# Optimization experiments

Measured on AMD Instinct MI355X. Metric: run time of the kernel, lower is better.

Reference implementation:

```python
import jax, jax.numpy as jnp
import numpy as np

B, L, CH = 8, 32768, 128   # segments, points per segment, channels
H, D = 4, 32               # num_head, ch_head (CH == H*D)
EPS = 1e-5                 # torch GroupNorm default eps


def group_norm1(x, w, b):
    # GroupNorm(num_groups=1, num_channels=CH) applied on [1, CH, L] per segment:
    # normalize over all channels AND points of each segment, then per-channel affine.
    mu = jnp.mean(x, axis=(1, 2), keepdims=True)            # [B,1,1]
    var = jnp.var(x, axis=(1, 2), keepdims=True)            # [B,1,1]
    return (x - mu) * jax.lax.rsqrt(var + EPS) * w + b      # [B,L,CH]


def setup_inputs() -> dict:
    key = jax.random.key(0)
    k0, k1, k2 = jax.random.split(key, 3)
    x = jax.random.normal(k0, (B, L, CH), dtype=jnp.float32)
    W_qkv = jax.random.normal(k1, (CH, 3 * H * D), dtype=jnp.float32) * 0.02
    W_out = jax.random.normal(k2, (H * D, CH), dtype=jnp.float32) * 0.02
    gn1_w = jnp.ones((CH,), jnp.float32)
    gn1_b = jnp.zeros((CH,), jnp.float32)
    gn2_w = jnp.ones((CH,), jnp.float32)
    gn2_b = jnp.zeros((CH,), jnp.float32)
    return {"x": x, "gn1_w": gn1_w, "gn1_b": gn1_b, "W_qkv": W_qkv,
            "W_out": W_out, "gn2_w": gn2_w, "gn2_b": gn2_b}


def reference(x, gn1_w, gn1_b, W_qkv, W_out, gn2_w, gn2_b):
    norm_x = group_norm1(x, gn1_w, gn1_b)                     # [B,L,CH]
    qkv = norm_x @ W_qkv                                      # [B,L,3*H*D]
    q, k, v = jnp.split(qkv, 3, axis=-1)
    q = q.reshape(B, L, H, D)
    k = k.reshape(B, L, H, D)
    v = v.reshape(B, L, H, D)
    # softmax over points within each segment (k / sqrt(segment_len))
    k_soft = jax.nn.softmax(k * (1.0 / np.float32(np.sqrt(L))), axis=1)
    # per-segment, per-head KV context: [B,H,D,D]
    context = jnp.einsum('blhk,blhv->bhkv', k_soft, v)
    # q scaled by ch_head**-0.5, softmax over feature dim
    q_soft = jax.nn.softmax(q * np.float32(D ** -0.5), axis=-1)
    out = jnp.einsum('blhk,bhkv->blhv', q_soft, context).reshape(B, L, H * D)
    out = out @ W_out                                          # [B,L,CH]
    out = group_norm1(out, gn2_w, gn2_b)
    return out + x  # residual
```

## Files before the change

kernel.cpp:

```cpp
#include <hip/hip_runtime.h>

#define NSEG 8
#define LSEG 32768
#define EPS_GN 1e-5f
#define KSCALE 0.005524271728019903f
#define QSCALE 0.17677669529663687f
#define INVN 2.384185791015625e-07f

typedef __attribute__((ext_vector_type(4))) float f32x4;
typedef __attribute__((ext_vector_type(8))) __bf16 bf16x8;
typedef __attribute__((ext_vector_type(4))) short s16x4;

#define MFMA32(A, B, C) __builtin_amdgcn_mfma_f32_16x16x32_bf16(A, B, C, 0, 0, 0)
#define MFMA16(A, B, C) __builtin_amdgcn_mfma_f32_16x16x16bf16_1k(A, B, C, 0, 0, 0)

static __device__ __forceinline__ unsigned short f2bf(float f) {
  unsigned int u = __float_as_uint(f);
  u += 0x7fffu + ((u >> 16) & 1u);
  return (unsigned short)(u >> 16);
}
static __device__ __forceinline__ float bf2f(unsigned short s) {
  return __uint_as_float(((unsigned int)s) << 16);
}
static __device__ __forceinline__ s16x4 pack4(float a, float b, float c, float d) {
  union { __bf16 h[4]; s16x4 s; } u;
  u.h[0] = (__bf16)a; u.h[1] = (__bf16)b; u.h[2] = (__bf16)c; u.h[3] = (__bf16)d;
  return u.s;
}

__global__ __launch_bounds__(256) void k_pre(
    const float* __restrict__ x, float* __restrict__ part, unsigned short* __restrict__ xb,
    const float* __restrict__ W, const float* __restrict__ gn1w, unsigned short* __restrict__ WT)
{
  const int t = threadIdx.x;
  if (blockIdx.x >= 512) {
    int idx = (blockIdx.x - 512) * 256 + t;
    int n = idx >> 7, ch = idx & 127;
    WT[idx] = f2bf(gn1w[ch] * W[ch * 384 + n]);
    return;
  }
  const int c = blockIdx.x;
  const float4* xp = (const float4*)x + (size_t)c * 16384;
  ushort4* xo = (ushort4*)xb + (size_t)c * 16384;
  float s = 0.f, q = 0.f;
  for (int i = 0; i < 64; ++i) {
    float4 v = xp[t + i * 256];
    s += v.x + v.y + v.z + v.w;
    q += v.x*v.x + v.y*v.y + v.z*v.z + v.w*v.w;
    xo[t + i * 256] = make_ushort4(f2bf(v.x), f2bf(v.y), f2bf(v.z), f2bf(v.w));
  }
  #pragma unroll
  for (int o = 1; o < 64; o <<= 1) { s += __shfl_xor(s, o); q += __shfl_xor(q, o); }
  __shared__ float red[8];
  int wave = t >> 6, lane = t & 63;
  if (lane == 0) { red[wave*2] = s; red[wave*2+1] = q; }
  __syncthreads();
  if (t == 0) {
    part[c*2]   = red[0] + red[2] + red[4] + red[6];
    part[c*2+1] = red[1] + red[3] + red[5] + red[7];
  }
}

__global__ __launch_bounds__(256, 2) void k_kv(
    const unsigned short* __restrict__ xb, const unsigned short* __restrict__ WT,
    const float* __restrict__ Wqkv, const float* __restrict__ gn1w, const float* __restrict__ gn1b,
    const float* __restrict__ part, float* __restrict__ sume_p, float* __restrict__ ctx_p)
{
  __shared__ float sm[2];
  __shared__ float sb01[512];
  __shared__ float sbias[256];

  const int t = threadIdx.x;
  const int h = t >> 6, lane = t & 63;
  const int lm = lane & 15, lg = lane >> 4;
  const int bid = blockIdx.x;
  const int seg = bid >> 6, sub = bid & 63;

  if (t < 64) {
    float s = part[(seg*64 + t)*2], q = part[(seg*64 + t)*2 + 1];
    #pragma unroll
    for (int o = 1; o < 64; o <<= 1) { s += __shfl_xor(s, o); q += __shfl_xor(q, o); }
    if (t == 0) {
      float mu = s * INVN;
      float var = q * INVN - mu * mu;
      float rs = rsqrtf(var + EPS_GN);
      sm[0] = mu * rs; sm[1] = rs;
    }
  }
  for (int p = t; p < 512; p += 256) {
    int which = p >> 8, n = 128 + (p & 255);
    const float* gv = which ? gn1w : gn1b;
    float s = 0.f;
    for (int ch = 0; ch < 128; ++ch) s += gv[ch] * Wqkv[ch*384 + n];
    sb01[p] = s;
  }
  __syncthreads();
  {
    float mu_rs = sm[0];
    int p = t;
    float v = sb01[p] - mu_rs * sb01[256 + p];
    sbias[p] = v * ((p < 128) ? KSCALE : 1.f);
  }
  __syncthreads();

  const float rs = sm[1];
  const float alk = rs * KSCALE, alv = rs;
  const float ck0 = sbias[h*32 + lm],       ck1 = sbias[h*32 + 16 + lm];
  const float cv0 = sbias[128 + h*32 + lm], cv1 = sbias[128 + h*32 + 16 + lm];

  bf16x8 wk[2][4], wv[2][4];
  #pragma unroll
  for (int nt = 0; nt < 2; ++nt)
    #pragma unroll
    for (int kk = 0; kk < 4; ++kk) {
      int row = h*32 + nt*16 + lm;
      wk[nt][kk] = *(const bf16x8*)&WT[(row + 128) * 128 + kk*32 + lg*8];
      wv[nt][kk] = *(const bf16x8*)&WT[(row + 256) * 128 + kk*32 + lg*8];
    }

  f32x4 ctx00 = {0,0,0,0}, ctx01 = {0,0,0,0}, ctx10 = {0,0,0,0}, ctx11 = {0,0,0,0};
  float se0 = 0.f, se1 = 0.f;

  const unsigned short* xw = xb + (size_t)(seg * LSEG + sub*512 + lm) * 128 + lg*8;

#define ISSUE(S, IT) { \
    const unsigned short* p_ = xw + (size_t)((IT) * 16) * 128; \
    S[0] = *(const bf16x8*)(p_);      \
    S[1] = *(const bf16x8*)(p_ + 32); \
    S[2] = *(const bf16x8*)(p_ + 64); \
    S[3] = *(const bf16x8*)(p_ + 96); }

#define COMPUTE(S) { \
    f32x4 ka0 = {0,0,0,0}, ka1 = {0,0,0,0}, va0 = {0,0,0,0}, va1 = {0,0,0,0}; \
    _Pragma("unroll") for (int kk = 0; kk < 4; ++kk) { \
      ka0 = MFMA32(S[kk], wk[0][kk], ka0); \
      ka1 = MFMA32(S[kk], wk[1][kk], ka1); \
    } \
    _Pragma("unroll") for (int kk = 0; kk < 4; ++kk) { \
      va0 = MFMA32(S[kk], wv[0][kk], va0); \
      va1 = MFMA32(S[kk], wv[1][kk], va1); \
    } \
    float e_[8]; \
    _Pragma("unroll") for (int r = 0; r < 4; ++r) { \
      e_[r]     = __expf(fmaf(ka0[r], alk, ck0)); \
      e_[4 + r] = __expf(fmaf(ka1[r], alk, ck1)); \
    } \
    se0 += (e_[0] + e_[1]) + (e_[2] + e_[3]); \
    se1 += (e_[4] + e_[5]) + (e_[6] + e_[7]); \
    s16x4 E0 = pack4(e_[0], e_[1], e_[2], e_[3]); \
    s16x4 E1 = pack4(e_[4], e_[5], e_[6], e_[7]); \
    s16x4 V0 = pack4(fmaf(va0[0], alv, cv0), fmaf(va0[1], alv, cv0), \
                     fmaf(va0[2], alv, cv0), fmaf(va0[3], alv, cv0)); \
    s16x4 V1 = pack4(fmaf(va1[0], alv, cv1), fmaf(va1[1], alv, cv1), \
                     fmaf(va1[2], alv, cv1), fmaf(va1[3], alv, cv1)); \
    ctx00 = MFMA16(E0, V0, ctx00); \
    ctx01 = MFMA16(E0, V1, ctx01); \
    ctx10 = MFMA16(E1, V0, ctx10); \
    ctx11 = MFMA16(E1, V1, ctx11); }

  bf16x8 sA[4], sB[4], sC[4], sD[4];
  ISSUE(sA, 0);
  ISSUE(sB, 1);
  #pragma unroll 1
  for (int it = 0; it < 32; it += 4) {
    ISSUE(sC, it + 2);
    COMPUTE(sA);
    ISSUE(sD, it + 3);
    COMPUTE(sB);
    if (it + 4 < 32) ISSUE(sA, it + 4);
    COMPUTE(sC);
    if (it + 5 < 32) ISSUE(sB, it + 5);
    COMPUTE(sD);
  }
#undef ISSUE
#undef COMPUTE

  se0 += __shfl_xor(se0, 16); se0 += __shfl_xor(se0, 32);
  se1 += __shfl_xor(se1, 16); se1 += __shfl_xor(se1, 32);
  if (lane < 16) {
    sume_p[(size_t)bid*128 + h*32 + lm]      = se0;
    sume_p[(size_t)bid*128 + h*32 + 16 + lm] = se1;
  }
  float* cp = ctx_p + (size_t)bid*4096 + h*1024;
  #pragma unroll
  for (int r = 0; r < 4; ++r) {
    cp[(lg*4 + r)*32      + lm]      = ctx00[r];
    cp[(lg*4 + r)*32      + 16 + lm] = ctx01[r];
    cp[(16 + lg*4 + r)*32 + lm]      = ctx10[r];
    cp[(16 + lg*4 + r)*32 + 16 + lm] = ctx11[r];
  }
}

__global__ __launch_bounds__(256) void k_wc(
    const float* __restrict__ sume_p, const float* __restrict__ ctx_p,
    const float* __restrict__ Wout, unsigned short* __restrict__ WcT)
{
  __shared__ float sctx[1024];
  __shared__ float sse[32];
  const int t = threadIdx.x, b = blockIdx.x;
  const int seg = b >> 5, head = (b >> 3) & 3, ocg = b & 7;
  float acc[4] = {0.f, 0.f, 0.f, 0.f};
  for (int j = 0; j < 64; ++j) {
    const float* cp = ctx_p + (size_t)(seg*64 + j)*4096 + head*1024;
    #pragma unroll
    for (int e = 0; e < 4; ++e) acc[e] += cp[t + e*256];
  }
  if (t < 32) {
    float s = 0.f;
    for (int j = 0; j < 64; ++j) s += sume_p[(size_t)(seg*64 + j)*128 + head*32 + t];
    sse[t] = s;
  }
  #pragma unroll
  for (int e = 0; e < 4; ++e) sctx[t + e*256] = acc[e];
  __syncthreads();
  #pragma unroll
  for (int e = 0; e < 2; ++e) {
    int idx = t + e*256;
    int kc = idx >> 4, ocl = idx & 15;
    int oc = ocg*16 + ocl;
    float s = 0.f;
    #pragma unroll
    for (int vc = 0; vc < 32; ++vc)
      s += sctx[kc*32 + vc] * Wout[(head*32 + vc)*128 + oc];
    WcT[((size_t)seg*128 + oc)*128 + head*32 + kc] = f2bf(s / sse[kc]);
  }
}

__global__ __launch_bounds__(256, 2) void k_out3(
    const unsigned short* __restrict__ xb, const unsigned short* __restrict__ WT,
    const float* __restrict__ Wqkv, const float* __restrict__ gn1w, const float* __restrict__ gn1b,
    const float* __restrict__ part, const unsigned short* __restrict__ WcT,
    float* __restrict__ part2, unsigned short* __restrict__ outm)
{
  __shared__ float sm[2];
  __shared__ float sb01[256];
  __shared__ float sbq[128];
  __shared__ float red[8];
  __shared__ __attribute__((aligned(16))) short pbuf[2][8 * 256];
  __shared__ __attribute__((aligned(16))) unsigned short sou[2][16 * 272];

  const int t = threadIdx.x;
  const int w = t >> 6, lane = t & 63;
  const int lm = lane & 15, lg = lane >> 4;
  const int bid = blockIdx.x;
  const int seg = bid >> 6;
  const size_t cb = (size_t)bid * 512;

  if (t < 64) {
    float s = part[(seg*64 + t)*2], q = part[(seg*64 + t)*2 + 1];
    #pragma unroll
    for (int o = 1; o < 64; o <<= 1) { s += __shfl_xor(s, o); q += __shfl_xor(q, o); }
    if (t == 0) {
      float mu = s * INVN;
      float var = q * INVN - mu * mu;
      float rs = rsqrtf(var + EPS_GN);
      sm[0] = mu * rs; sm[1] = rs;
    }
  }
  {
    int which = t >> 7, n = t & 127;
    const float* gv = which ? gn1w : gn1b;
    float s = 0.f;
    for (int ch = 0; ch < 128; ++ch) s += gv[ch] * Wqkv[ch*384 + n];
    sb01[t] = s;
  }
  __syncthreads();
  if (t < 128) sbq[t] = (sb01[t] - sm[0] * sb01[128 + t]) * QSCALE;
  __syncthreads();

  const float alq = sm[1] * QSCALE;
  const float4 cq0 = *(const float4*)&sbq[w*32 + lg*4];
  const float4 cq1 = *(const float4*)&sbq[w*32 + 16 + lg*4];

  bf16x8 wq[2][4];
  #pragma unroll
  for (int nt = 0; nt < 2; ++nt)
    #pragma unroll
    for (int kk = 0; kk < 4; ++kk)
      wq[nt][kk] = *(const bf16x8*)&WT[(w*32 + nt*16 + lm) * 128 + kk*32 + lg*8];
  s16x4 wc[2][8];
  #pragma unroll
  for (int o = 0; o < 2; ++o)
    #pragma unroll
    for (int kt = 0; kt < 8; ++kt)
      wc[o][kt] = *(const s16x4*)&WcT[((size_t)seg*128 + (w*32 + o*16 + lm))*128 + kt*16 + lg*4];

  const unsigned short* xw = xb + (cb + lm) * 128 + lg*8;
  float ssum = 0.f, ssq = 0.f;

  #pragma unroll 1
  for (int ia = 0; ia < 32; ++ia) {
    const unsigned short* p_ = xw + (size_t)(ia * 16) * 128;
    bf16x8 xf0 = *(const bf16x8*)(p_);
    bf16x8 xf1 = *(const bf16x8*)(p_ + 32);
    bf16x8 xf2 = *(const bf16x8*)(p_ + 64);
    bf16x8 xf3 = *(const bf16x8*)(p_ + 96);
    f32x4 qa0 = {0,0,0,0}, qa1 = {0,0,0,0};
    qa0 = MFMA32(wq[0][0], xf0, qa0); qa1 = MFMA32(wq[1][0], xf0, qa1);
    qa0 = MFMA32(wq[0][1], xf1, qa0); qa1 = MFMA32(wq[1][1], xf1, qa1);
    qa0 = MFMA32(wq[0][2], xf2, qa0); qa1 = MFMA32(wq[1][2], xf2, qa1);
    qa0 = MFMA32(wq[0][3], xf3, qa0); qa1 = MFMA32(wq[1][3], xf3, qa1);
    float a[8];
    #pragma unroll
    for (int r = 0; r < 4; ++r) {
      a[r]     = fmaf(qa0[r], alq, ((const float*)&cq0)[r]);
      a[4 + r] = fmaf(qa1[r], alq, ((const float*)&cq1)[r]);
    }
    float m = a[0];
    #pragma unroll
    for (int i = 1; i < 8; ++i) m = fmaxf(m, a[i]);
    m = fmaxf(m, __shfl_xor(m, 16));
    m = fmaxf(m, __shfl_xor(m, 32));
    float s = 0.f;
    #pragma unroll
    for (int i = 0; i < 8; ++i) { a[i] = __expf(a[i] - m); s += a[i]; }
    s += __shfl_xor(s, 16);
    s += __shfl_xor(s, 32);
    float inv = 1.f / s;
    *(s16x4*)&pbuf[ia & 1][(w*2)*256 + lane*4]     = pack4(a[0]*inv, a[1]*inv, a[2]*inv, a[3]*inv);
    *(s16x4*)&pbuf[ia & 1][(w*2 + 1)*256 + lane*4] = pack4(a[4]*inv, a[5]*inv, a[6]*inv, a[7]*inv);
    __syncthreads();
    f32x4 acc0 = {0,0,0,0}, acc1 = {0,0,0,0};
    #pragma unroll
    for (int kt = 0; kt < 8; ++kt) {
      s16x4 pk = *(const s16x4*)&pbuf[ia & 1][kt*256 + lane*4];
      acc0 = MFMA16(wc[0][kt], pk, acc0);
      acc1 = MFMA16(wc[1][kt], pk, acc1);
    }
    #pragma unroll
    for (int r = 0; r < 4; ++r) {
      ssum += acc0[r] + acc1[r];
      ssq  += acc0[r]*acc0[r] + acc1[r]*acc1[r];
    }
    {
      unsigned short* dst = &sou[ia & 1][lm*272 + w*32 + lg*4];
      dst[0] = f2bf(acc0[0]); dst[1] = f2bf(acc0[1]);
      dst[2] = f2bf(acc0[2]); dst[3] = f2bf(acc0[3]);
      dst += 16;
      dst[0] = f2bf(acc1[0]); dst[1] = f2bf(acc1[1]);
      dst[2] = f2bf(acc1[2]); dst[3] = f2bf(acc1[3]);
    }
    __syncthreads();
    #pragma unroll
    for (int j = 0; j < 2; ++j) {
      int f = t + j*256;
      int pt = f >> 5, cc = f & 31;
      ((ushort4*)outm)[(cb + (size_t)ia*16 + pt)*32 + cc] = *(const ushort4*)&sou[ia & 1][pt*272 + cc*4];
    }
  }

  #pragma unroll
  for (int o = 1; o < 64; o <<= 1) { ssum += __shfl_xor(ssum, o); ssq += __shfl_xor(ssq, o); }
  if (lane == 0) { red[w*2] = ssum; red[w*2+1] = ssq; }
  __syncthreads();
  if (t == 0) {
    part2[bid*2]   = red[0] + red[2] + red[4] + red[6];
    part2[bid*2+1] = red[1] + red[3] + red[5] + red[7];
  }
}

__global__ __launch_bounds__(256) void k_fin(
    const unsigned short* __restrict__ xb, const unsigned short* __restrict__ out_ws,
    const float* __restrict__ part2, const float* __restrict__ gn2w, const float* __restrict__ gn2b,
    float* __restrict__ y)
{
  __shared__ float sm[2];
  const int t = threadIdx.x;
  const int b = blockIdx.x >> 8, blk = blockIdx.x & 255;
  if (t < 64) {
    float s = part2[(b*64 + t)*2], q = part2[(b*64 + t)*2 + 1];
    #pragma unroll
    for (int o = 1; o < 64; o <<= 1) { s += __shfl_xor(s, o); q += __shfl_xor(q, o); }
    if (t == 0) {
      float mu = s * INVN;
      float var = q * INVN - mu * mu;
      sm[0] = mu; sm[1] = rsqrtf(var + EPS_GN);
    }
  }
  __syncthreads();
  const float mu = sm[0], rs = sm[1];
  const int c4 = t & 31;
  const float4 w4 = *(const float4*)&gn2w[c4*4];
  const float4 g4 = *(const float4*)&gn2b[c4*4];
  const size_t base = (size_t)b * 1048576 + (size_t)blk * 4096;
  const ushort4* xp = (const ushort4*)xb + base;
  const ushort4* op = (const ushort4*)out_ws + base;
  float4* yp = (float4*)y + base;
  #pragma unroll
  for (int i = 0; i < 16; ++i) {
    int f = t + i * 256;
    ushort4 xv = xp[f];
    ushort4 ov = op[f];
    float4 r;
    r.x = (bf2f(ov.x) - mu) * rs * w4.x + g4.x + bf2f(xv.x);
    r.y = (bf2f(ov.y) - mu) * rs * w4.y + g4.y + bf2f(xv.y);
    r.z = (bf2f(ov.z) - mu) * rs * w4.z + g4.z + bf2f(xv.z);
    r.w = (bf2f(ov.w) - mu) * rs * w4.w + g4.w + bf2f(xv.w);
    yp[f] = r;
  }
}

extern "C" void kernel_launch(void* const* d_in, const int* in_sizes, int n_in,
                              void* d_out, int out_size, void* d_ws, size_t ws_size,
                              hipStream_t stream) {
  const float* x    = (const float*)d_in[0];
  const float* gn1w = (const float*)d_in[1];
  const float* gn1b = (const float*)d_in[2];
  const float* Wqkv = (const float*)d_in[3];
  const float* Wout = (const float*)d_in[4];
  const float* gn2w = (const float*)d_in[5];
  const float* gn2b = (const float*)d_in[6];
  float* y = (float*)d_out;
  char* ws = (char*)d_ws;

  float*          part   = (float*)(ws + 0);
  float*          part2  = (float*)(ws + 4096);
  unsigned short* WT     = (unsigned short*)(ws + 8192);
  unsigned short* WcT    = (unsigned short*)(ws + 106496);
  float*          sume_p = (float*)(ws + 368640);
  float*          ctx_p  = (float*)(ws + 630784);
  unsigned short* xb     = (unsigned short*)(ws + 9019392);
  unsigned short* outm   = (unsigned short*)(ws + 76128256);

  hipLaunchKernelGGL(k_pre,  dim3(704),  dim3(256), 0, stream, x, part, xb, Wqkv, gn1w, WT);
  hipLaunchKernelGGL(k_kv,   dim3(512),  dim3(256), 0, stream, xb, WT, Wqkv, gn1w, gn1b, part, sume_p, ctx_p);
  hipLaunchKernelGGL(k_wc,   dim3(256),  dim3(256), 0, stream, sume_p, ctx_p, Wout, WcT);
  hipLaunchKernelGGL(k_out3, dim3(512),  dim3(256), 0, stream, xb, WT, Wqkv, gn1w, gn1b, part, WcT, part2, outm);
  hipLaunchKernelGGL(k_fin,  dim3(2048), dim3(256), 0, stream, xb, outm, part2, gn2w, gn2b, y);
}
```

Measured before the change: 213.9 us.

## Software-pipeline k_out3 loop with one barrier per step, shrink k_kv prefetch depth

```diff
diff --git a/kernel.cpp b/kernel.cpp
--- a/kernel.cpp
+++ b/kernel.cpp
@@ -6,6 +6,7 @@
 #define KSCALE 0.005524271728019903f
 #define QSCALE 0.17677669529663687f
 #define INVN 2.384185791015625e-07f
+#define SOPITCH 260
 
 typedef __attribute__((ext_vector_type(4))) float f32x4;
 typedef __attribute__((ext_vector_type(8))) __bf16 bf16x8;
@@ -26,6 +27,11 @@
   union { __bf16 h[4]; s16x4 s; } u;
   u.h[0] = (__bf16)a; u.h[1] = (__bf16)b; u.h[2] = (__bf16)c; u.h[3] = (__bf16)d;
   return u.s;
+}
+static __device__ __forceinline__ ushort4 cvt4(float4 v) {
+  union { __bf16 h[4]; ushort4 u; } z;
+  z.h[0] = (__bf16)v.x; z.h[1] = (__bf16)v.y; z.h[2] = (__bf16)v.z; z.h[3] = (__bf16)v.w;
+  return z.u;
 }
 
 __global__ __launch_bounds__(256) void k_pre(
@@ -43,11 +49,12 @@
   const float4* xp = (const float4*)x + (size_t)c * 16384;
   ushort4* xo = (ushort4*)xb + (size_t)c * 16384;
   float s = 0.f, q = 0.f;
+  #pragma unroll 8
   for (int i = 0; i < 64; ++i) {
     float4 v = xp[t + i * 256];
     s += v.x + v.y + v.z + v.w;
     q += v.x*v.x + v.y*v.y + v.z*v.z + v.w*v.w;
-    xo[t + i * 256] = make_ushort4(f2bf(v.x), f2bf(v.y), f2bf(v.z), f2bf(v.w));
+    xo[t + i * 256] = cvt4(v);
   }
   #pragma unroll
   for (int o = 1; o < 64; o <<= 1) { s += __shfl_xor(s, o); q += __shfl_xor(q, o); }
@@ -158,19 +165,14 @@
     ctx10 = MFMA16(E1, V0, ctx10); \
     ctx11 = MFMA16(E1, V1, ctx11); }
 
-  bf16x8 sA[4], sB[4], sC[4], sD[4];
+  bf16x8 sA[4], sB[4];
   ISSUE(sA, 0);
-  ISSUE(sB, 1);
   #pragma unroll 1
-  for (int it = 0; it < 32; it += 4) {
-    ISSUE(sC, it + 2);
+  for (int it = 0; it < 32; it += 2) {
+    ISSUE(sB, it + 1);
     COMPUTE(sA);
-    ISSUE(sD, it + 3);
+    if (it + 2 < 32) ISSUE(sA, it + 2);
     COMPUTE(sB);
-    if (it + 4 < 32) ISSUE(sA, it + 4);
-    COMPUTE(sC);
-    if (it + 5 < 32) ISSUE(sB, it + 5);
-    COMPUTE(sD);
   }
 #undef ISSUE
 #undef COMPUTE
@@ -237,7 +239,7 @@
   __shared__ float sbq[128];
   __shared__ float red[8];
   __shared__ __attribute__((aligned(16))) short pbuf[2][8 * 256];
-  __shared__ __attribute__((aligned(16))) unsigned short sou[2][16 * 272];
+  __shared__ __attribute__((aligned(16))) unsigned short sou[2][16 * SOPITCH];
 
   const int t = threadIdx.x;
   const int w = t >> 6, lane = t & 63;
@@ -287,45 +289,61 @@
 
   const unsigned short* xw = xb + (cb + lm) * 128 + lg*8;
   float ssum = 0.f, ssq = 0.f;
+  bf16x8 xf0, xf1, xf2, xf3;
+
+#define LOADXF(IT) { \
+    const unsigned short* p_ = xw + (size_t)((IT) * 16) * 128; \
+    xf0 = *(const bf16x8*)(p_);      \
+    xf1 = *(const bf16x8*)(p_ + 32); \
+    xf2 = *(const bf16x8*)(p_ + 64); \
+    xf3 = *(const bf16x8*)(p_ + 96); }
+
+#define SM2P(D) { \
+    f32x4 qa0 = {0,0,0,0}, qa1 = {0,0,0,0}; \
+    qa0 = MFMA32(wq[0][0], xf0, qa0); qa1 = MFMA32(wq[1][0], xf0, qa1); \
+    qa0 = MFMA32(wq[0][1], xf1, qa0); qa1 = MFMA32(wq[1][1], xf1, qa1); \
+    qa0 = MFMA32(wq[0][2], xf2, qa0); qa1 = MFMA32(wq[1][2], xf2, qa1); \
+    qa0 = MFMA32(wq[0][3], xf3, qa0); qa1 = MFMA32(wq[1][3], xf3, qa1); \
+    float a_[8]; \
+    _Pragma("unroll") for (int r = 0; r < 4; ++r) { \
+      a_[r]     = fmaf(qa0[r], alq, ((const float*)&cq0)[r]); \
+      a_[4 + r] = fmaf(qa1[r], alq, ((const float*)&cq1)[r]); \
+    } \
+    float m_ = a_[0]; \
+    _Pragma("unroll") for (int i = 1; i < 8; ++i) m_ = fmaxf(m_, a_[i]); \
+    m_ = fmaxf(m_, __shfl_xor(m_, 16)); \
+    m_ = fmaxf(m_, __shfl_xor(m_, 32)); \
+    float s_ = 0.f; \
+    _Pragma("unroll") for (int i = 0; i < 8; ++i) { a_[i] = __expf(a_[i] - m_); s_ += a_[i]; } \
+    s_ += __shfl_xor(s_, 16); \
+    s_ += __shfl_xor(s_, 32); \
+    float inv_ = 1.f / s_; \
+    *(s16x4*)&pbuf[D][(w*2)*256 + lane*4]     = pack4(a_[0]*inv_, a_[1]*inv_, a_[2]*inv_, a_[3]*inv_); \
+    *(s16x4*)&pbuf[D][(w*2 + 1)*256 + lane*4] = pack4(a_[4]*inv_, a_[5]*inv_, a_[6]*inv_, a_[7]*inv_); }
+
+  LOADXF(0);
+  SM2P(0);
 
   #pragma unroll 1
   for (int ia = 0; ia < 32; ++ia) {
-    const unsigned short* p_ = xw + (size_t)(ia * 16) * 128;
-    bf16x8 xf0 = *(const bf16x8*)(p_);
-    bf16x8 xf1 = *(const bf16x8*)(p_ + 32);
-    bf16x8 xf2 = *(const bf16x8*)(p_ + 64);
-    bf16x8 xf3 = *(const bf16x8*)(p_ + 96);
-    f32x4 qa0 = {0,0,0,0}, qa1 = {0,0,0,0};
-    qa0 = MFMA32(wq[0][0], xf0, qa0); qa1 = MFMA32(wq[1][0], xf0, qa1);
-    qa0 = MFMA32(wq[0][1], xf1, qa0); qa1 = MFMA32(wq[1][1], xf1, qa1);
-    qa0 = MFMA32(wq[0][2], xf2, qa0); qa1 = MFMA32(wq[1][2], xf2, qa1);
-    qa0 = MFMA32(wq[0][3], xf3, qa0); qa1 = MFMA32(wq[1][3], xf3, qa1);
-    float a[8];
-    #pragma unroll
-    for (int r = 0; r < 4; ++r) {
-      a[r]     = fmaf(qa0[r], alq, ((const float*)&cq0)[r]);
-      a[4 + r] = fmaf(qa1[r], alq, ((const float*)&cq1)[r]);
-    }
-    float m = a[0];
-    #pragma unroll
-    for (int i = 1; i < 8; ++i) m = fmaxf(m, a[i]);
-    m = fmaxf(m, __shfl_xor(m, 16));
-    m = fmaxf(m, __shfl_xor(m, 32));
-    float s = 0.f;
-    #pragma unroll
-    for (int i = 0; i < 8; ++i) { a[i] = __expf(a[i] - m); s += a[i]; }
-    s += __shfl_xor(s, 16);
-    s += __shfl_xor(s, 32);
-    float inv = 1.f / s;
-    *(s16x4*)&pbuf[ia & 1][(w*2)*256 + lane*4]     = pack4(a[0]*inv, a[1]*inv, a[2]*inv, a[3]*inv);
-    *(s16x4*)&pbuf[ia & 1][(w*2 + 1)*256 + lane*4] = pack4(a[4]*inv, a[5]*inv, a[6]*inv, a[7]*inv);
+    const int d = ia & 1;
     __syncthreads();
+    if (ia + 1 < 32) LOADXF(ia + 1);
     f32x4 acc0 = {0,0,0,0}, acc1 = {0,0,0,0};
     #pragma unroll
     for (int kt = 0; kt < 8; ++kt) {
-      s16x4 pk = *(const s16x4*)&pbuf[ia & 1][kt*256 + lane*4];
+      s16x4 pk = *(const s16x4*)&pbuf[d][kt*256 + lane*4];
       acc0 = MFMA16(wc[0][kt], pk, acc0);
       acc1 = MFMA16(wc[1][kt], pk, acc1);
+    }
+    if (ia > 0) {
+      #pragma unroll
+      for (int j = 0; j < 2; ++j) {
+        int f = t + j*256;
+        int pt = f >> 5, cc = f & 31;
+        ((ushort4*)outm)[(cb + (size_t)(ia-1)*16 + pt)*32 + cc] =
+            *(const ushort4*)&sou[d^1][pt*SOPITCH + cc*4];
+      }
     }
     #pragma unroll
     for (int r = 0; r < 4; ++r) {
@@ -333,21 +351,25 @@
       ssq  += acc0[r]*acc0[r] + acc1[r]*acc1[r];
     }
     {
-      unsigned short* dst = &sou[ia & 1][lm*272 + w*32 + lg*4];
+      unsigned short* dst = &sou[d][lm*SOPITCH + w*32 + lg*4];
       dst[0] = f2bf(acc0[0]); dst[1] = f2bf(acc0[1]);
       dst[2] = f2bf(acc0[2]); dst[3] = f2bf(acc0[3]);
       dst += 16;
       dst[0] = f2bf(acc1[0]); dst[1] = f2bf(acc1[1]);
       dst[2] = f2bf(acc1[2]); dst[3] = f2bf(acc1[3]);
     }
-    __syncthreads();
-    #pragma unroll
-    for (int j = 0; j < 2; ++j) {
-      int f = t + j*256;
-      int pt = f >> 5, cc = f & 31;
-      ((ushort4*)outm)[(cb + (size_t)ia*16 + pt)*32 + cc] = *(const ushort4*)&sou[ia & 1][pt*272 + cc*4];
-    }
-  }
+    if (ia + 1 < 32) SM2P(d ^ 1);
+  }
+  __syncthreads();
+  #pragma unroll
+  for (int j = 0; j < 2; ++j) {
+    int f = t + j*256;
+    int pt = f >> 5, cc = f & 31;
+    ((ushort4*)outm)[(cb + (size_t)31*16 + pt)*32 + cc] =
+        *(const ushort4*)&sou[1][pt*SOPITCH + cc*4];
+  }
+#undef LOADXF
+#undef SM2P
 
   #pragma unroll
   for (int o = 1; o < 64; o <<= 1) { ssum += __shfl_xor(ssum, o); ssq += __shfl_xor(ssq, o); }
```

Result: slower. 218.2 us (+2.0%).
